# Kernel tuning notes

Hardware: AMD Instinct MI355X
Metric: run time of the kernel (lower is better)

## Reference

```python
import jax, jax.numpy as jnp
import numpy as np

H = 4          # num attention heads
LRELU = 0.2    # DGL GATConv leaky-relu slope
N_GT, N_AG = 100000, 20000
E_GT, E_COMM = 640000, 320000
D_GT, D_AG = 32, 64
VIS, COMM, MSG, OUT = 64, 128, 64, 5
NUM_COMM_STEPS = 2


def _leaky(x):
    return jnp.where(x >= 0, x, LRELU * x)


def gat(feat_src, feat_dst, w_src, w_dst, a_l, a_r, bias, src, dst, n_dst, dh):
    """Bipartite DGL GATConv: residual=Identity (in_dst == H*dh), activation=ReLU."""
    fs = (feat_src @ w_src).reshape(-1, H, dh)   # [Ns,H,dh]
    fd = (feat_dst @ w_dst).reshape(-1, H, dh)   # [Nd,H,dh]
    el = (fs * a_l[None]).sum(-1)                # [Ns,H]
    er = (fd * a_r[None]).sum(-1)                # [Nd,H]
    e = _leaky(el[src] + er[dst])                # [E,H]
    emax = jax.ops.segment_max(e, dst, num_segments=n_dst)
    ex = jnp.exp(e - emax[dst])
    denom = jax.ops.segment_sum(ex, dst, num_segments=n_dst)
    a = ex / denom[dst]                          # edge softmax over in-edges
    rst = jax.ops.segment_sum(fs[src] * a[..., None], dst, num_segments=n_dst)
    rst = rst + feat_dst.reshape(n_dst, H, dh)   # identity residual
    rst = rst + bias.reshape(1, H, dh)
    return jax.nn.relu(rst).reshape(n_dst, H * dh)


def gru(x, h, w_ih, w_hh, b_ih, b_hh):
    gi = x @ w_ih + b_ih
    gh = h @ w_hh + b_hh
    i_r, i_z, i_n = jnp.split(gi, 3, axis=1)
    h_r, h_z, h_n = jnp.split(gh, 3, axis=1)
    r = jax.nn.sigmoid(i_r + h_r)
    zg = jax.nn.sigmoid(i_z + h_z)
    n = jnp.tanh(i_n + r * h_n)
    return (1.0 - zg) * n + zg * h


def setup_inputs() -> dict:
    key = jax.random.key(0)
    ks = jax.random.split(key, 32)
    def w(k, shp):
        return (jax.random.normal(k, shp, dtype=jnp.float32) / np.sqrt(shp[0])).astype(jnp.float32)
    dh1, dh2 = VIS // H, COMM // H
    inp = {
        'feat_gt': jax.random.normal(ks[0], (N_GT, D_GT), dtype=jnp.float32),
        'feat_agent': jax.random.normal(ks[1], (N_AG, D_AG), dtype=jnp.float32),
        'z': jax.random.normal(ks[2], (N_AG, COMM), dtype=jnp.float32),
        'gt_src': jax.random.randint(ks[3], (E_GT,), 0, N_GT, dtype=jnp.int32),
        'gt_dst': jax.random.randint(ks[4], (E_GT,), 0, N_AG, dtype=jnp.int32),
        'comm_src': jax.random.randint(ks[5], (E_COMM,), 0, N_AG, dtype=jnp.int32),
        'comm_dst': jax.random.randint(ks[6], (E_COMM,), 0, N_AG, dtype=jnp.int32),
        # vis1 GATConv (gt->agent), out 64 = 4 heads x 16
        'w1_src': w(ks[7], (D_GT, VIS)), 'w1_dst': w(ks[8], (D_AG, VIS)),
        'a1_l': w(ks[9], (H, dh1)), 'a1_r': w(ks[10], (H, dh1)),
        'b1': jnp.zeros((VIS,), jnp.float32),
        'w2_src': w(ks[11], (D_GT, COMM)), 'w2_dst': w(ks[12], (VIS + D_AG, COMM)),
        'a2_l': w(ks[13], (H, dh2)), 'a2_r': w(ks[14], (H, dh2)),
        'b2': jnp.zeros((COMM,), jnp.float32),
        # comm f_enc: mlp([128,128,64]) with ReLU everywhere
        'enc_w1': w(ks[15], (COMM, 128)), 'enc_b1': jnp.zeros((128,), jnp.float32),
        'enc_w2': w(ks[16], (128, MSG)), 'enc_b2': jnp.zeros((MSG,), jnp.float32),
        # GRUCell(in=COMM+MSG=192, hidden=COMM=128), stored [in, 3*hidden]
        'gru_w_ih': w(ks[17], (COMM + MSG, 3 * COMM)),
        'gru_w_hh': w(ks[18], (COMM, 3 * COMM)),
        'gru_b_ih': jnp.zeros((3 * COMM,), jnp.float32),
        'gru_b_hh': jnp.zeros((3 * COMM,), jnp.float32),
        # f_out
        'out_w': w(ks[19], (COMM, OUT)), 'out_b': jnp.zeros((OUT,), jnp.float32),
    }
    return inp


def _forward(feat_gt, feat_agent, z, gt_src, gt_dst, comm_src, comm_dst,
             w1_src, w1_dst, a1_l, a1_r, b1,
             w2_src, w2_dst, a2_l, a2_r, b2,
             enc_w1, enc_b1, enc_w2, enc_b2,
             gru_w_ih, gru_w_hh, gru_b_ih, gru_b_hh,
             out_w, out_b):
    n_ag = feat_agent.shape[0]
    h_vis1 = gat(feat_gt, feat_agent, w1_src, w1_dst, a1_l, a1_r, b1,
                 gt_src, gt_dst, n_ag, VIS // H)
    dst2 = jnp.concatenate([h_vis1, feat_agent], axis=1)
    h = gat(feat_gt, dst2, w2_src, w2_dst, a2_l, a2_r, b2,
            gt_src, gt_dst, n_ag, COMM // H)
    deg = jax.ops.segment_sum(jnp.ones_like(comm_dst, dtype=jnp.float32),
                              comm_dst, num_segments=n_ag)
    denom = jnp.maximum(deg, 1.0)[:, None]
    zz = z
    for _ in range(NUM_COMM_STEPS):
        m = jax.nn.relu(jax.nn.relu(h @ enc_w1 + enc_b1) @ enc_w2 + enc_b2)  # per-node f_enc
        y = jax.ops.segment_sum(m[comm_src], comm_dst, num_segments=n_ag) / denom  # mailbox mean
        h = gru(jnp.concatenate([h, y], axis=1), zz, gru_w_ih, gru_w_hh, gru_b_ih, gru_b_hh)
        zz = h
    h_out = h @ out_w + out_b
    return h_out, zz


def reference(feat_gt, feat_agent, z, gt_src, gt_dst, comm_src, comm_dst,
              w1_src, w1_dst, a1_l, a1_r, b1,
              w2_src, w2_dst, a2_l, a2_r, b2,
              enc_w1, enc_b1, enc_w2, enc_b2,
              gru_w_ih, gru_w_hh, gru_b_ih, gru_b_hh,
              out_w, out_b):
    return _forward(feat_gt, feat_agent, z, gt_src, gt_dst, comm_src, comm_dst,
                    w1_src, w1_dst, a1_l, a1_r, b1,
                    w2_src, w2_dst, a2_l, a2_r, b2,
                    enc_w1, enc_b1, enc_w2, enc_b2,
                    gru_w_ih, gru_w_hh, gru_b_ih, gru_b_hh,
                    out_w, out_b)
```

## Files before the change

### kernel.cpp

```cpp
#include <hip/hip_runtime.h>
#include <math.h>

#define NHEAD 4
#define LRELU_S 0.2f
constexpr int N_GT = 100000, N_AG = 20000;
constexpr int E_GT = 640000, E_COMM = 320000;
constexpr int OUTD = 5;
constexpr int NBLK_SC = (N_AG + 255) / 256;
constexpr int MB_GT = (N_GT + 63) / 64;
constexpr int FS_TILES = 3 * MB_GT;
constexpr int ETILES  = (N_AG + 31) / 32;
constexpr int GGROUPS = (N_AG + 3) / 4;

constexpr long O_CNTP_GT = 0;
constexpr long O_CNTP_CM = 320000;
constexpr long O_FSB1    = 0;
constexpr long O_FSB2    = 3200000;
constexpr long O_EL1     = 12800000;
constexpr long O_EL2     = 13200000;
constexpr long O_ER1     = 14880000;
constexpr long O_RST2    = 17600000;
constexpr long O_DINV    = 20160000;
constexpr long O_OFFS_GT = 20180000;
constexpr long O_SRT_GT  = 20200004;
constexpr long O_OFFS_CM = 20840004;
constexpr long O_SRT_CM  = 20860008;
constexpr long O_PART    = 21180008;
constexpr long O_V       = 21220008;
constexpr long O_WB      = 21300000;
constexpr long O_RANK_GT = 21500000;
constexpr long O_RANK_CM = 22140000;
constexpr long O_M  = 10240000;
constexpr long O_Y  = 15360000;

constexpr long WB_FS  = 0;
constexpr long WB_E1  = 6144;
constexpr long WB_E2  = 22528;
constexpr long WB_RZ  = 30720;
constexpr long WB_GIN = 112640;
constexpr long WB_GHN = 137216;

using bf8      = __attribute__((ext_vector_type(8))) short;
using f32x4v   = __attribute__((ext_vector_type(4))) float;
using ushort8v = __attribute__((ext_vector_type(8))) unsigned short;

__device__ __forceinline__ unsigned short f2bf(float x) {
    unsigned u = __float_as_uint(x);
    u += 0x7FFFu + ((u >> 16) & 1u);
    return (unsigned short)(u >> 16);
}
__device__ __forceinline__ float bf2f(unsigned short u) {
    return __uint_as_float(((unsigned)u) << 16);
}

__global__ __launch_bounds__(256) void p0_k(
    const float* __restrict__ w1s, const float* __restrict__ w1d,
    const float* __restrict__ a1l, const float* __restrict__ a1r,
    const float* __restrict__ w2s, const float* __restrict__ w2d,
    const float* __restrict__ a2l, const float* __restrict__ a2r,
    const float* __restrict__ e1, const float* __restrict__ e2,
    const float* __restrict__ gih, const float* __restrict__ ghh,
    float* __restrict__ ws)
{
    const int tid = (int)(blockIdx.x * 256 + threadIdx.x);
    const int NT  = (int)(gridDim.x * 256);
    unsigned* wsu = reinterpret_cast<unsigned*>(ws);
    unsigned short* wb = reinterpret_cast<unsigned short*>(ws + O_WB);
    for (int i = tid; i < 640000; i += NT) wsu[O_CNTP_GT + i] = 0u;
    for (int i = tid; i < 153600; i += NT) {
        float val;
        if (i < 2048)        { long l = i;          long n = l / 32,  k = l % 32;  val = w1s[k * 64 + n]; }
        else if (i < 6144)   { long l = i - 2048;   long n = l / 32,  k = l % 32;  val = w2s[k * 128 + n]; }
        else if (i < 22528)  { long l = i - 6144;   long n = l / 128, k = l % 128; val = e1[k * 128 + n]; }
        else if (i < 30720)  { long l = i - 22528;  long n = l / 128, k = l % 128; val = e2[k * 64 + n]; }
        else if (i < 112640) { long l = i - 30720;  long n = l / 320, k = l % 320;
                               val = (k < 192) ? gih[k * 384 + n] : ghh[(k - 192) * 384 + n]; }
        else if (i < 137216) { long l = i - 112640; long n = l / 192, k = l % 192; val = gih[k * 384 + 256 + n]; }
        else                 { long l = i - 137216; long n = l / 128, k = l % 128; val = ghh[k * 384 + 256 + n]; }
        wb[i] = f2bf(val);
    }
    if (tid < 1024) {
        const int i = tid;
        const float *wp, *ap; int dh, local;
        if (i < 128)      { wp = w1s; ap = a1l; dh = 16; local = i; }
        else if (i < 384) { wp = w1d; ap = a1r; dh = 16; local = i - 128; }
        else if (i < 512) { wp = w2s; ap = a2l; dh = 32; local = i - 384; }
        else              { wp = w2d; ap = a2r; dh = 32; local = i - 512; }
        int k = local >> 2, hh = local & 3;
        float s = 0.f;
        for (int j = 0; j < dh; ++j) s += wp[k * (4 * dh) + hh * dh + j] * ap[hh * dh + j];
        ws[O_V + i] = s;
    }
}

__global__ __launch_bounds__(256) void p1_k(
    const int* __restrict__ gt_dst, const int* __restrict__ comm_dst,
    const float* __restrict__ feat_gt, const float* __restrict__ feat_agent,
    float* __restrict__ ws)
{
    const int tid = (int)(blockIdx.x * 256 + threadIdx.x);
    unsigned* wsu = reinterpret_cast<unsigned*>(ws);
    if (tid < E_GT) {
        wsu[O_RANK_GT + tid] = atomicAdd(wsu + O_CNTP_GT + (long)gt_dst[tid] * 16, 1u);
    } else if (tid < E_GT + E_COMM) {
        int j = tid - E_GT;
        wsu[O_RANK_CM + j] = atomicAdd(wsu + O_CNTP_CM + (long)comm_dst[j] * 16, 1u);
    }
    const float* v1  = ws + O_V;
    const float* v2  = ws + O_V + 384;
    const float* vr1 = ws + O_V + 128;
    float* el1 = ws + O_EL1;
    float* el2 = ws + O_EL2;
    float* er1 = ws + O_ER1;
    if (tid < N_GT) {
        const int i = tid;
        float a[8] = {};
        const float* fp = feat_gt + (long)i * 32;
        for (int k = 0; k < 32; ++k) {
            float x = fp[k];
#pragma unroll
            for (int j = 0; j < 4; ++j) a[j] += x * v1[4 * k + j];
#pragma unroll
            for (int j = 0; j < 4; ++j) a[4 + j] += x * v2[4 * k + j];
        }
        *reinterpret_cast<float4*>(el1 + 4l * i) = {a[0], a[1], a[2], a[3]};
        *reinterpret_cast<float4*>(el2 + 4l * i) = {a[4], a[5], a[6], a[7]};
    } else if (tid < N_GT + N_AG) {
        int r = tid - N_GT;
        float a0 = 0, a1 = 0, a2 = 0, a3 = 0;
        const float* fp = feat_agent + (long)r * 64;
        for (int k = 0; k < 64; ++k) {
            float x = fp[k];
            a0 += x * vr1[4 * k];     a1 += x * vr1[4 * k + 1];
            a2 += x * vr1[4 * k + 2]; a3 += x * vr1[4 * k + 3];
        }
        *reinterpret_cast<float4*>(er1 + 4l * r) = {a0, a1, a2, a3};
    }
}

__global__ __launch_bounds__(256) void p2_k(float* __restrict__ ws)
{
    __shared__ unsigned shu[256];
    unsigned* wsu = reinterpret_cast<unsigned*>(ws);
    const int b = (int)blockIdx.x, t = (int)threadIdx.x;
    const int g  = (b >= NBLK_SC) ? 1 : 0;
    const int cb = b - g * NBLK_SC;
    const int i  = cb * 256 + t;
    const unsigned* cnt = wsu + (g ? O_CNTP_CM : O_CNTP_GT);
    unsigned c = (i < N_AG) ? cnt[(long)i * 16] : 0u;
    if (g && i < N_AG) ws[O_DINV + i] = 1.0f / fmaxf((float)c, 1.0f);
    shu[t] = c;
    __syncthreads();
    for (int off = 1; off < 256; off <<= 1) {
        unsigned v = (t >= off) ? shu[t - off] : 0u;
        __syncthreads();
        shu[t] += v;
        __syncthreads();
    }
    unsigned* offs = wsu + (g ? O_OFFS_CM : O_OFFS_GT);
    if (i < N_AG) offs[i] = shu[t] - c;
    if (t == 255) wsu[O_PART + b] = shu[255];
}

__global__ __launch_bounds__(256) void p3_k(float* __restrict__ ws)
{
    __shared__ unsigned shu[128];
    unsigned* wsu = reinterpret_cast<unsigned*>(ws);
    const int b = (int)blockIdx.x, t = (int)threadIdx.x;
    const int g  = (b >= NBLK_SC) ? 1 : 0;
    const int cb = b - g * NBLK_SC;
    if (t < 128) shu[t] = (t < cb) ? wsu[O_PART + g * NBLK_SC + t] : 0u;
    __syncthreads();
    for (int off = 64; off >= 1; off >>= 1) {
        if (t < off) shu[t] += shu[t + off];
        __syncthreads();
    }
    const unsigned pre = shu[0];
    unsigned* offs = wsu + (g ? O_OFFS_CM : O_OFFS_GT);
    const int i = cb * 256 + t;
    if (i < N_AG) offs[i] += pre;
    if (b == NBLK_SC - 1 && t == 0)     wsu[O_OFFS_GT + N_AG] = E_GT;
    if (b == 2 * NBLK_SC - 1 && t == 0) wsu[O_OFFS_CM + N_AG] = E_COMM;
}

__global__ __launch_bounds__(256) void p4_k(
    const int* __restrict__ gt_src, const int* __restrict__ gt_dst,
    const int* __restrict__ comm_src, const int* __restrict__ comm_dst,
    const float* __restrict__ A, float* __restrict__ ws)
{
    unsigned* wsu = reinterpret_cast<unsigned*>(ws);
    const int t = (int)threadIdx.x;
    const int tid = (int)(blockIdx.x * 256 + t);
    if (tid < E_GT) {
        wsu[O_SRT_GT + wsu[O_OFFS_GT + gt_dst[tid]] + wsu[O_RANK_GT + tid]] = (unsigned)gt_src[tid];
    } else if (tid < E_GT + E_COMM) {
        int j = tid - E_GT;
        wsu[O_SRT_CM + wsu[O_OFFS_CM + comm_dst[j]] + wsu[O_RANK_CM + j]] = (unsigned)comm_src[j];
    }

    __shared__ __align__(16) unsigned short As[64][40];
    __shared__ __align__(16) unsigned short Bs[64][40];
    const unsigned short* Btc = reinterpret_cast<unsigned short*>(ws + O_WB) + WB_FS;
    unsigned short* fsb1 = reinterpret_cast<unsigned short*>(ws + O_FSB1);
    unsigned short* fsb2 = reinterpret_cast<unsigned short*>(ws + O_FSB2);
    const int lane = t & 63, wv = t >> 6;
    const int wm = wv & 1, wn = wv >> 1;
    const int quad = lane >> 4, l16 = lane & 15;
    const int rA = t >> 3, cA = (t & 7) * 4;
    const int rB = t >> 2, cB = (t & 3) * 8;
    const int tt = (int)blockIdx.x;
    if (tt >= FS_TILES) return;
    const int n0 = (tt % 3) * 64, m0 = (tt / 3) * 64;
#pragma unroll
    for (int half = 0; half < 2; ++half) {
        const int r = rA + half * 32;
        const int row = m0 + r;
        float4 v = {0.f, 0.f, 0.f, 0.f};
        if (row < N_GT) v = *reinterpret_cast<const float4*>(A + (long)row * 32 + cA);
        ushort4 bb;
        bb.x = f2bf(v.x); bb.y = f2bf(v.y); bb.z = f2bf(v.z); bb.w = f2bf(v.w);
        *reinterpret_cast<ushort4*>(&As[r][cA]) = bb;
    }
    *reinterpret_cast<ushort8v*>(&Bs[rB][cB]) =
        *reinterpret_cast<const ushort8v*>(Btc + (long)(n0 + rB) * 32 + cB);
    __syncthreads();
    f32x4v acc[2][2] = {};
    const bf8 a0 = *reinterpret_cast<const bf8*>(&As[wm * 32 + l16][quad * 8]);
    const bf8 a1 = *reinterpret_cast<const bf8*>(&As[wm * 32 + 16 + l16][quad * 8]);
    const bf8 b0v = *reinterpret_cast<const bf8*>(&Bs[wn * 32 + l16][quad * 8]);
    const bf8 b1v = *reinterpret_cast<const bf8*>(&Bs[wn * 32 + 16 + l16][quad * 8]);
    acc[0][0] = __builtin_amdgcn_mfma_f32_16x16x32_bf16(a0, b0v, acc[0][0], 0, 0, 0);
    acc[0][1] = __builtin_amdgcn_mfma_f32_16x16x32_bf16(a0, b1v, acc[0][1], 0, 0, 0);
    acc[1][0] = __builtin_amdgcn_mfma_f32_16x16x32_bf16(a1, b0v, acc[1][0], 0, 0, 0);
    acc[1][1] = __builtin_amdgcn_mfma_f32_16x16x32_bf16(a1, b1v, acc[1][1], 0, 0, 0);
#pragma unroll
    for (int mt = 0; mt < 2; ++mt)
#pragma unroll
        for (int nt = 0; nt < 2; ++nt)
#pragma unroll
            for (int r = 0; r < 4; ++r) {
                const int row = m0 + wm * 32 + mt * 16 + quad * 4 + r;
                const int col = n0 + wn * 32 + nt * 16 + l16;
                if (row < N_GT) {
                    unsigned short v16 = f2bf(acc[mt][nt][r]);
                    if (col < 64) fsb1[(long)row * 64 + col] = v16;
                    else          fsb2[(long)row * 128 + (col - 64)] = v16;
                }
            }
}

__global__ __launch_bounds__(256) void gat12_k(
    const unsigned* __restrict__ offs, const unsigned* __restrict__ ssrc,
    const float* __restrict__ el1, const float* __restrict__ er1,
    const float* __restrict__ el2,
    const unsigned short* __restrict__ fsb1, const unsigned short* __restrict__ fsb2,
    const float* __restrict__ feat_agent,
    const float* __restrict__ b1, const float* __restrict__ b2,
    const float* __restrict__ vr2, float* __restrict__ out)
{
    const int wid = threadIdx.x >> 6, lane = threadIdx.x & 63;
    const int d = blockIdx.x * 4 + wid;
    if (d >= N_AG) return;
    const int h = lane >> 4, ei = lane & 15;
    const unsigned beg = offs[d], end = offs[d + 1];
    const unsigned smax = (unsigned)N_GT - 1u;

    float m = -INFINITY, s = 0.f, acc0 = 0.f;
    {
        const float er_h = er1[4l * d + h];
        for (unsigned base = beg; base < end; base += 16) {
            const unsigned na = min(16u, end - base);
            unsigned sv = ssrc[base + ((unsigned)ei < na ? (unsigned)ei : 0u)];
            sv = min(sv, smax);
            unsigned short fw[16];
#pragma unroll
            for (int j = 0; j < 16; ++j) {
                const unsigned sj = (unsigned)__shfl((int)sv, j);
                fw[j] = fsb1[(long)sj * 64 + lane];
            }
            float xv = -INFINITY;
            if ((unsigned)ei < na) {
                float x = el1[4l * sv + h] + er_h;
                xv = (x >= 0.f) ? x : LRELU_S * x;
            }
            float cm = xv;
#pragma unroll
            for (int off = 1; off < 16; off <<= 1) cm = fmaxf(cm, __shfl_xor(cm, off));
            const float mn = fmaxf(m, cm);
            const float corr = __expf(m - mn);
            const float p = __expf(xv - mn);
            float ps = p;
#pragma unroll
            for (int off = 1; off < 16; off <<= 1) ps += __shfl_xor(ps, off);
            s = s * corr + ps;
            acc0 *= corr;
            m = mn;
#pragma unroll
            for (int j = 0; j < 16; ++j) {
                const float pj = __shfl(p, (h << 4) | j);
                acc0 += pj * bf2f(fw[j]);
            }
        }
    }
    const float inv1 = (s > 0.f) ? 1.f / s : 0.f;
    const float r1 = feat_agent[(long)d * 64 + lane];
    const float o = fmaxf(acc0 * inv1 + r1 + b1[lane], 0.f);

    float e0 = o * vr2[lane * 4 + 0] + r1 * vr2[(64 + lane) * 4 + 0];
    float e1v = o * vr2[lane * 4 + 1] + r1 * vr2[(64 + lane) * 4 + 1];
    float e2v = o * vr2[lane * 4 + 2] + r1 * vr2[(64 + lane) * 4 + 2];
    float e3v = o * vr2[lane * 4 + 3] + r1 * vr2[(64 + lane) * 4 + 3];
#pragma unroll
    for (int off = 1; off < 64; off <<= 1) {
        e0  += __shfl_xor(e0, off);
        e1v += __shfl_xor(e1v, off);
        e2v += __shfl_xor(e2v, off);
        e3v += __shfl_xor(e3v, off);
    }
    const float er_h2 = (h == 0) ? e0 : (h == 1) ? e1v : (h == 2) ? e2v : e3v;

    const int c0 = lane * 2;
    float m2 = -INFINITY, s2 = 0.f, A0 = 0.f, A1 = 0.f;
    for (unsigned base = beg; base < end; base += 16) {
        const unsigned na = min(16u, end - base);
        unsigned sv = ssrc[base + ((unsigned)ei < na ? (unsigned)ei : 0u)];
        sv = min(sv, smax);
        unsigned fw[16];
#pragma unroll
        for (int j = 0; j < 16; ++j) {
            const unsigned sj = (unsigned)__shfl((int)sv, j);
            fw[j] = *reinterpret_cast<const unsigned*>(fsb2 + (long)sj * 128 + c0);
        }
        float xv = -INFINITY;
        if ((unsigned)ei < na) {
            float x = el2[4l * sv + h] + er_h2;
            xv = (x >= 0.f) ? x : LRELU_S * x;
        }
        float cm = xv;
#pragma unroll
        for (int off = 1; off < 16; off <<= 1) cm = fmaxf(cm, __shfl_xor(cm, off));
        const float mn = fmaxf(m2, cm);
        const float corr = __expf(m2 - mn);
        const float p = __expf(xv - mn);
        float ps = p;
#pragma unroll
        for (int off = 1; off < 16; off <<= 1) ps += __shfl_xor(ps, off);
        s2 = s2 * corr + ps;
        A0 *= corr; A1 *= corr;
        m2 = mn;
#pragma unroll
        for (int j = 0; j < 16; ++j) {
            const float pj = __shfl(p, (h << 4) | j);
            A0 += pj * __uint_as_float((fw[j] & 0xFFFFu) << 16);
            A1 += pj * __uint_as_float((fw[j] >> 16) << 16);
        }
    }
    const float inv2 = (s2 > 0.f) ? 1.f / s2 : 0.f;
    const float rox = __shfl(o, c0 & 63);
    const float roy = __shfl(o, (c0 + 1) & 63);
    float2 r;
    if (c0 < 64) { r.x = rox; r.y = roy; }
    else r = *reinterpret_cast<const float2*>(feat_agent + (long)d * 64 + (c0 - 64));
    float2 oo;
    oo.x = fmaxf(A0 * inv2 + r.x + b2[c0], 0.f);
    oo.y = fmaxf(A1 * inv2 + r.y + b2[c0 + 1], 0.f);
    *reinterpret_cast<float2*>(out + (long)d * 128 + c0) = oo;
}

__global__ __launch_bounds__(256) void enc_k(
    const float* __restrict__ h,
    const unsigned short* __restrict__ we1, const unsigned short* __restrict__ we2,
    const float* __restrict__ eb1, const float* __restrict__ eb2,
    unsigned short* __restrict__ mb)
{
    __shared__ __align__(16) unsigned short U[8704];
    const int tid = (int)threadIdx.x;
    const int lane = tid & 63, w = tid >> 6;
    const int quad = lane >> 4, l16 = lane & 15;
    const int m0 = (int)blockIdx.x * 32;
#pragma unroll
    for (int it = 0; it < 4; ++it) {
        int idx = tid + it * 256;
        int row = idx >> 5, cc = (idx & 31) * 4;
        int grow = m0 + row;
        float4 v = {0.f, 0.f, 0.f, 0.f};
        if (grow < N_AG) v = *reinterpret_cast<const float4*>(h + (long)grow * 128 + cc);
        ushort4 bb;
        bb.x = f2bf(v.x); bb.y = f2bf(v.y); bb.z = f2bf(v.z); bb.w = f2bf(v.w);
        *reinterpret_cast<ushort4*>(&U[row * 136 + cc]) = bb;
    }
    __syncthreads();
#pragma unroll 1
    for (int jg = w; jg < 8; jg += 4) {
        const int j0 = jg * 16;
        const unsigned short* p = we1 + (long)(j0 + l16) * 128 + quad * 8;
        bf8 bw[4];
#pragma unroll
        for (int i2 = 0; i2 < 4; ++i2) bw[i2] = *reinterpret_cast<const bf8*>(p + i2 * 32);
        f32x4v acc[2] = {};
#pragma unroll
        for (int i2 = 0; i2 < 4; ++i2) {
            const int k0 = i2 * 32;
            const bf8 a0 = *reinterpret_cast<const bf8*>(&U[l16 * 136 + k0 + quad * 8]);
            const bf8 a1 = *reinterpret_cast<const bf8*>(&U[(16 + l16) * 136 + k0 + quad * 8]);
            acc[0] = __builtin_amdgcn_mfma_f32_16x16x32_bf16(a0, bw[i2], acc[0], 0, 0, 0);
            acc[1] = __builtin_amdgcn_mfma_f32_16x16x32_bf16(a1, bw[i2], acc[1], 0, 0, 0);
        }
        const int j = j0 + l16;
        const float bj = eb1[j];
#pragma unroll
        for (int mt = 0; mt < 2; ++mt)
#pragma unroll
            for (int r = 0; r < 4; ++r)
                U[4352 + (mt * 16 + quad * 4 + r) * 136 + j] = f2bf(fmaxf(acc[mt][r] + bj, 0.f));
    }
    __syncthreads();
    {
        const int j0 = w * 16;
        if (w < 4) {
            const unsigned short* p = we2 + (long)(j0 + l16) * 128 + quad * 8;
            bf8 bw[4];
#pragma unroll
            for (int i2 = 0; i2 < 4; ++i2) bw[i2] = *reinterpret_cast<const bf8*>(p + i2 * 32);
            f32x4v acc[2] = {};
#pragma unroll
            for (int i2 = 0; i2 < 4; ++i2) {
                const int k0 = i2 * 32;
                const bf8 a0 = *reinterpret_cast<const bf8*>(&U[4352 + l16 * 136 + k0 + quad * 8]);
                const bf8 a1 = *reinterpret_cast<const bf8*>(&U[4352 + (16 + l16) * 136 + k0 + quad * 8]);
                acc[0] = __builtin_amdgcn_mfma_f32_16x16x32_bf16(a0, bw[i2], acc[0], 0, 0, 0);
                acc[1] = __builtin_amdgcn_mfma_f32_16x16x32_bf16(a1, bw[i2], acc[1], 0, 0, 0);
            }
            const int j = j0 + l16;
            const float bj = eb2[j];
#pragma unroll
            for (int mt = 0; mt < 2; ++mt)
#pragma unroll
                for (int r = 0; r < 4; ++r) {
                    const int row = m0 + mt * 16 + quad * 4 + r;
                    if (row < N_AG)
                        mb[(long)row * 64 + j] = f2bf(fmaxf(acc[mt][r] + bj, 0.f));
                }
        }
    }
}

__global__ __launch_bounds__(256) void gather_k(
    const unsigned* __restrict__ coffs, const unsigned* __restrict__ cssrc,
    const unsigned short* __restrict__ mb, const float* __restrict__ dinv,
    float* __restrict__ y)
{
    const int tid = (int)threadIdx.x;
    const int lane = tid & 63, w = tid >> 6;
    const int d = (int)blockIdx.x * 4 + w;
    if (d >= N_AG) return;
    const unsigned beg = coffs[d], endo = coffs[d + 1];
    const int ei = lane & 15;
    float acc = 0.f;
    for (unsigned base = beg; base < endo; base += 16) {
        const unsigned na = min(16u, endo - base);
        unsigned sv = cssrc[base + ((unsigned)ei < na ? (unsigned)ei : 0u)];
        sv = min(sv, (unsigned)(N_AG - 1));
        unsigned short fw[16];
#pragma unroll
        for (int j = 0; j < 16; ++j) {
            const unsigned sj = (unsigned)__shfl((int)sv, j);
            fw[j] = mb[(long)sj * 64 + lane];
        }
#pragma unroll
        for (int j = 0; j < 16; ++j)
            if ((unsigned)j < na) acc += bf2f(fw[j]);
    }
    y[(long)d * 64 + lane] = acc * dinv[d];
}

__global__ __launch_bounds__(256) void gru_k(
    const float* __restrict__ h_in, const float* __restrict__ y, const float* zz,
    const unsigned short* __restrict__ wrz, const unsigned short* __restrict__ wgin,
    const unsigned short* __restrict__ wghn,
    const float* __restrict__ gbih, const float* __restrict__ gbhh,
    float* hout)
{
    __shared__ __align__(16) unsigned short U[32 * 328];
    const int tid = (int)threadIdx.x;
    const int lane = tid & 63, w = tid >> 6;
    const int quad = lane >> 4, l16 = lane & 15;
    const int m0 = (int)blockIdx.x * 32;
#pragma unroll
    for (int it = 0; it < 10; ++it) {
        int idx = tid + it * 256;
        int row = idx / 80, cc = (idx - row * 80) * 4;
        int grow = m0 + row;
        float4 v = {0.f, 0.f, 0.f, 0.f};
        if (grow < N_AG) {
            if (cc < 128)      v = *reinterpret_cast<const float4*>(h_in + (long)grow * 128 + cc);
            else if (cc < 192) v = *reinterpret_cast<const float4*>(y + (long)grow * 64 + (cc - 128));
            else               v = *reinterpret_cast<const float4*>(zz + (long)grow * 128 + (cc - 192));
        }
        ushort4 bb;
        bb.x = f2bf(v.x); bb.y = f2bf(v.y); bb.z = f2bf(v.z); bb.w = f2bf(v.w);
        *reinterpret_cast<ushort4*>(&U[row * 328 + cc]) = bb;
    }
    __syncthreads();
#pragma unroll 1
    for (int jg = w; jg < 8; jg += 4) {
        const int j0 = jg * 16;
        f32x4v aR[2] = {}, aZ[2] = {}, aI[2] = {}, aH[2] = {};
        {
            const unsigned short* pR = wrz + (long)(j0 + l16) * 320 + quad * 8;
            const unsigned short* pZ = wrz + (long)(128 + j0 + l16) * 320 + quad * 8;
#pragma unroll
            for (int half = 0; half < 2; ++half) {
                bf8 bR[5], bZ[5];
#pragma unroll
                for (int i2 = 0; i2 < 5; ++i2) {
                    const int k0 = half * 160 + i2 * 32;
                    bR[i2] = *reinterpret_cast<const bf8*>(pR + k0);
                    bZ[i2] = *reinterpret_cast<const bf8*>(pZ + k0);
                }
#pragma unroll
                for (int i2 = 0; i2 < 5; ++i2) {
                    const int k0 = half * 160 + i2 * 32;
                    const bf8 a0 = *reinterpret_cast<const bf8*>(&U[l16 * 328 + k0 + quad * 8]);
                    const bf8 a1 = *reinterpret_cast<const bf8*>(&U[(16 + l16) * 328 + k0 + quad * 8]);
                    aR[0] = __builtin_amdgcn_mfma_f32_16x16x32_bf16(a0, bR[i2], aR[0], 0, 0, 0);
                    aR[1] = __builtin_amdgcn_mfma_f32_16x16x32_bf16(a1, bR[i2], aR[1], 0, 0, 0);
                    aZ[0] = __builtin_amdgcn_mfma_f32_16x16x32_bf16(a0, bZ[i2], aZ[0], 0, 0, 0);
                    aZ[1] = __builtin_amdgcn_mfma_f32_16x16x32_bf16(a1, bZ[i2], aZ[1], 0, 0, 0);
                }
            }
        }
        {
            const unsigned short* pI = wgin + (long)(j0 + l16) * 192 + quad * 8;
            bf8 bI[6];
#pragma unroll
            for (int i2 = 0; i2 < 6; ++i2) bI[i2] = *reinterpret_cast<const bf8*>(pI + i2 * 32);
#pragma unroll
            for (int i2 = 0; i2 < 6; ++i2) {
                const int k0 = i2 * 32;
                const bf8 a0 = *reinterpret_cast<const bf8*>(&U[l16 * 328 + k0 + quad * 8]);
                const bf8 a1 = *reinterpret_cast<const bf8*>(&U[(16 + l16) * 328 + k0 + quad * 8]);
                aI[0] = __builtin_amdgcn_mfma_f32_16x16x32_bf16(a0, bI[i2], aI[0], 0, 0, 0);
                aI[1] = __builtin_amdgcn_mfma_f32_16x16x32_bf16(a1, bI[i2], aI[1], 0, 0, 0);
            }
        }
        {
            const unsigned short* pH = wghn + (long)(j0 + l16) * 128 + quad * 8;
            bf8 bH[4];
#pragma unroll
            for (int i2 = 0; i2 < 4; ++i2) bH[i2] = *reinterpret_cast<const bf8*>(pH + i2 * 32);
#pragma unroll
            for (int i2 = 0; i2 < 4; ++i2) {
                const int k0 = 192 + i2 * 32;
                const bf8 a0 = *reinterpret_cast<const bf8*>(&U[l16 * 328 + k0 + quad * 8]);
                const bf8 a1 = *reinterpret_cast<const bf8*>(&U[(16 + l16) * 328 + k0 + quad * 8]);
                aH[0] = __builtin_amdgcn_mfma_f32_16x16x32_bf16(a0, bH[i2], aH[0], 0, 0, 0);
                aH[1] = __builtin_amdgcn_mfma_f32_16x16x32_bf16(a1, bH[i2], aH[1], 0, 0, 0);
            }
        }
        const int j = j0 + l16;
#pragma unroll
        for (int mt = 0; mt < 2; ++mt)
#pragma unroll
            for (int r = 0; r < 4; ++r) {
                const int row = m0 + mt * 16 + quad * 4 + r;
                if (row >= N_AG) continue;
                const float rr = 1.f / (1.f + __expf(-(aR[mt][r] + gbih[j] + gbhh[j])));
                const float zg = 1.f / (1.f + __expf(-(aZ[mt][r] + gbih[128 + j] + gbhh[128 + j])));
                const float nn = tanhf(aI[mt][r] + gbih[256 + j] + rr * (aH[mt][r] + gbhh[256 + j]));
                const float hp = zz[(long)row * 128 + j];
                hout[(long)row * 128 + j] = (1.f - zg) * nn + zg * hp;
            }
    }
}

__global__ __launch_bounds__(256) void out_k(
    const float* __restrict__ h, const float* __restrict__ ow,
    const float* __restrict__ ob, float* __restrict__ out)
{
    const int gtid = (int)(blockIdx.x * 256 + threadIdx.x);
    float4* od = reinterpret_cast<float4*>(out + (long)N_AG * OUTD);
    const float4* hs = reinterpret_cast<const float4*>(h);
    if (gtid < N_AG * 32) od[gtid] = hs[gtid];
    if (gtid < N_AG) {
        float acc[OUTD];
#pragma unroll
        for (int j = 0; j < OUTD; ++j) acc[j] = ob[j];
        for (int k = 0; k < 128; ++k) {
            float v = h[(long)gtid * 128 + k];
#pragma unroll
            for (int j = 0; j < OUTD; ++j) acc[j] += v * ow[k * OUTD + j];
        }
#pragma unroll
        for (int j = 0; j < OUTD; ++j) out[(long)gtid * OUTD + j] = acc[j];
    }
}

extern "C" void kernel_launch(void* const* d_in, const int* in_sizes, int n_in,
                              void* d_out, int out_size, void* d_ws, size_t ws_size,
                              hipStream_t stream) {
    const float* feat_gt    = (const float*)d_in[0];
    const float* feat_agent = (const float*)d_in[1];
    const float* z_in       = (const float*)d_in[2];
    const int*   gt_src     = (const int*)d_in[3];
    const int*   gt_dst     = (const int*)d_in[4];
    const int*   comm_src   = (const int*)d_in[5];
    const int*   comm_dst   = (const int*)d_in[6];
    const float* w1_src = (const float*)d_in[7];
    const float* w1_dst = (const float*)d_in[8];
    const float* a1_l   = (const float*)d_in[9];
    const float* a1_r   = (const float*)d_in[10];
    const float* b1     = (const float*)d_in[11];
    const float* w2_src = (const float*)d_in[12];
    const float* w2_dst = (const float*)d_in[13];
    const float* a2_l   = (const float*)d_in[14];
    const float* a2_r   = (const float*)d_in[15];
    const float* b2     = (const float*)d_in[16];
    const float* enc_w1 = (const float*)d_in[17];
    const float* enc_b1 = (const float*)d_in[18];
    const float* enc_w2 = (const float*)d_in[19];
    const float* enc_b2 = (const float*)d_in[20];
    const float* gw_ih  = (const float*)d_in[21];
    const float* gw_hh  = (const float*)d_in[22];
    const float* gb_ih  = (const float*)d_in[23];
    const float* gb_hh  = (const float*)d_in[24];
    const float* out_w  = (const float*)d_in[25];
    const float* out_b  = (const float*)d_in[26];

    float* ws = (float*)d_ws;
    unsigned* wsu = (unsigned*)d_ws;
    unsigned short* wb = (unsigned short*)(ws + O_WB);
    float* out = (float*)d_out;

    float* hptr = ws + O_RST2;
    unsigned short* mb = (unsigned short*)(ws + O_M);
    float* yb = ws + O_Y;

    p0_k<<<dim3(2500), dim3(256), 0, stream>>>(w1_src, w1_dst, a1_l, a1_r,
                                               w2_src, w2_dst, a2_l, a2_r,
                                               enc_w1, enc_w2, gw_ih, gw_hh, ws);
    p1_k<<<dim3(3750), dim3(256), 0, stream>>>(gt_dst, comm_dst, feat_gt, feat_agent, ws);
    p2_k<<<dim3(2 * NBLK_SC), dim3(256), 0, stream>>>(ws);
    p3_k<<<dim3(2 * NBLK_SC), dim3(256), 0, stream>>>(ws);
    p4_k<<<dim3(FS_TILES), dim3(256), 0, stream>>>(gt_src, gt_dst, comm_src, comm_dst,
                                                   feat_gt, ws);

    gat12_k<<<dim3(GGROUPS), dim3(256), 0, stream>>>(
        wsu + O_OFFS_GT, wsu + O_SRT_GT,
        ws + O_EL1, ws + O_ER1, ws + O_EL2,
        (const unsigned short*)(ws + O_FSB1), (const unsigned short*)(ws + O_FSB2),
        feat_agent, b1, b2, ws + O_V + 512, hptr);

    for (int step = 0; step < 2; ++step) {
        const float* zz = (step == 0) ? z_in : hptr;
        enc_k<<<dim3(ETILES), dim3(256), 0, stream>>>(hptr, wb + WB_E1, wb + WB_E2,
                                                      enc_b1, enc_b2, mb);
        gather_k<<<dim3(GGROUPS), dim3(256), 0, stream>>>(wsu + O_OFFS_CM, wsu + O_SRT_CM,
                                                          mb, ws + O_DINV, yb);
        gru_k<<<dim3(ETILES), dim3(256), 0, stream>>>(hptr, yb, zz, wb + WB_RZ, wb + WB_GIN,
                                                      wb + WB_GHN, gb_ih, gb_hh, hptr);
    }
    out_k<<<dim3(2500), dim3(256), 0, stream>>>(hptr, out_w, out_b, out);
}
```

Baseline: 411.1 us.

## Process 32 edges per iteration in gathers and widen enc/gru blocks to 512

The GAT and mailbox gather loops now handle two 16-edge chunks per iteration, issuing both sets of feature loads before the online-softmax update so more memory requests are in flight and fewer reductions run per edge. The encoder and GRU kernels move to 512-thread blocks, with each of the 8 waves owning one 16-column slice instead of looping over two. This aims to hide gather latency and raise wave parallelism, at the cost of more registers per thread, which may lower occupancy.

```diff
diff --git a/kernel.cpp b/kernel.cpp
--- a/kernel.cpp
+++ b/kernel.cpp
@@ -268,28 +268,48 @@
     float m = -INFINITY, s = 0.f, acc0 = 0.f;
     {
         const float er_h = er1[4l * d + h];
-        for (unsigned base = beg; base < end; base += 16) {
-            const unsigned na = min(16u, end - base);
-            unsigned sv = ssrc[base + ((unsigned)ei < na ? (unsigned)ei : 0u)];
-            sv = min(sv, smax);
-            unsigned short fw[16];
+        for (unsigned base = beg; base < end; base += 32) {
+            const unsigned rem = end - base;
+            const unsigned naA = min(16u, rem);
+            const bool hasB = rem > 16u;
+            unsigned svA = ssrc[base + ((unsigned)ei < naA ? (unsigned)ei : 0u)];
+            svA = min(svA, smax);
+            unsigned svB = 0u; unsigned naB = 0u;
+            if (hasB) {
+                naB = min(16u, rem - 16u);
+                svB = ssrc[base + 16u + ((unsigned)ei < naB ? (unsigned)ei : 0u)];
+                svB = min(svB, smax);
+            }
+            unsigned short fwA[16], fwB[16];
 #pragma unroll
             for (int j = 0; j < 16; ++j) {
-                const unsigned sj = (unsigned)__shfl((int)sv, j);
-                fw[j] = fsb1[(long)sj * 64 + lane];
-            }
-            float xv = -INFINITY;
-            if ((unsigned)ei < na) {
-                float x = el1[4l * sv + h] + er_h;
-                xv = (x >= 0.f) ? x : LRELU_S * x;
-            }
-            float cm = xv;
+                const unsigned sj = (unsigned)__shfl((int)svA, j);
+                fwA[j] = fsb1[(long)sj * 64 + lane];
+            }
+            if (hasB) {
+#pragma unroll
+                for (int j = 0; j < 16; ++j) {
+                    const unsigned sj = (unsigned)__shfl((int)svB, j);
+                    fwB[j] = fsb1[(long)sj * 64 + lane];
+                }
+            }
+            float xvA = -INFINITY, xvB = -INFINITY;
+            if ((unsigned)ei < naA) {
+                float x = el1[4l * svA + h] + er_h;
+                xvA = (x >= 0.f) ? x : LRELU_S * x;
+            }
+            if (hasB && (unsigned)ei < naB) {
+                float x = el1[4l * svB + h] + er_h;
+                xvB = (x >= 0.f) ? x : LRELU_S * x;
+            }
+            float cm = fmaxf(xvA, xvB);
 #pragma unroll
             for (int off = 1; off < 16; off <<= 1) cm = fmaxf(cm, __shfl_xor(cm, off));
             const float mn = fmaxf(m, cm);
             const float corr = __expf(m - mn);
-            const float p = __expf(xv - mn);
-            float ps = p;
+            const float pA = __expf(xvA - mn);
+            const float pB = __expf(xvB - mn);
+            float ps = pA + pB;
 #pragma unroll
             for (int off = 1; off < 16; off <<= 1) ps += __shfl_xor(ps, off);
             s = s * corr + ps;
@@ -297,8 +317,15 @@
             m = mn;
 #pragma unroll
             for (int j = 0; j < 16; ++j) {
-                const float pj = __shfl(p, (h << 4) | j);
-                acc0 += pj * bf2f(fw[j]);
+                const float pj = __shfl(pA, (h << 4) | j);
+                acc0 += pj * bf2f(fwA[j]);
+            }
+            if (hasB) {
+#pragma unroll
+                for (int j = 0; j < 16; ++j) {
+                    const float pj = __shfl(pB, (h << 4) | j);
+                    acc0 += pj * bf2f(fwB[j]);
+                }
             }
         }
     }
@@ -321,28 +348,48 @@
 
     const int c0 = lane * 2;
     float m2 = -INFINITY, s2 = 0.f, A0 = 0.f, A1 = 0.f;
-    for (unsigned base = beg; base < end; base += 16) {
-        const unsigned na = min(16u, end - base);
-        unsigned sv = ssrc[base + ((unsigned)ei < na ? (unsigned)ei : 0u)];
-        sv = min(sv, smax);
-        unsigned fw[16];
+    for (unsigned base = beg; base < end; base += 32) {
+        const unsigned rem = end - base;
+        const unsigned naA = min(16u, rem);
+        const bool hasB = rem > 16u;
+        unsigned svA = ssrc[base + ((unsigned)ei < naA ? (unsigned)ei : 0u)];
+        svA = min(svA, smax);
+        unsigned svB = 0u; unsigned naB = 0u;
+        if (hasB) {
+            naB = min(16u, rem - 16u);
+            svB = ssrc[base + 16u + ((unsigned)ei < naB ? (unsigned)ei : 0u)];
+            svB = min(svB, smax);
+        }
+        unsigned fwA[16], fwB[16];
 #pragma unroll
         for (int j = 0; j < 16; ++j) {
-            const unsigned sj = (unsigned)__shfl((int)sv, j);
-            fw[j] = *reinterpret_cast<const unsigned*>(fsb2 + (long)sj * 128 + c0);
-        }
-        float xv = -INFINITY;
-        if ((unsigned)ei < na) {
-            float x = el2[4l * sv + h] + er_h2;
-            xv = (x >= 0.f) ? x : LRELU_S * x;
-        }
-        float cm = xv;
+            const unsigned sj = (unsigned)__shfl((int)svA, j);
+            fwA[j] = *reinterpret_cast<const unsigned*>(fsb2 + (long)sj * 128 + c0);
+        }
+        if (hasB) {
+#pragma unroll
+            for (int j = 0; j < 16; ++j) {
+                const unsigned sj = (unsigned)__shfl((int)svB, j);
+                fwB[j] = *reinterpret_cast<const unsigned*>(fsb2 + (long)sj * 128 + c0);
+            }
+        }
+        float xvA = -INFINITY, xvB = -INFINITY;
+        if ((unsigned)ei < naA) {
+            float x = el2[4l * svA + h] + er_h2;
+            xvA = (x >= 0.f) ? x : LRELU_S * x;
+        }
+        if (hasB && (unsigned)ei < naB) {
+            float x = el2[4l * svB + h] + er_h2;
+            xvB = (x >= 0.f) ? x : LRELU_S * x;
+        }
+        float cm = fmaxf(xvA, xvB);
 #pragma unroll
         for (int off = 1; off < 16; off <<= 1) cm = fmaxf(cm, __shfl_xor(cm, off));
         const float mn = fmaxf(m2, cm);
         const float corr = __expf(m2 - mn);
-        const float p = __expf(xv - mn);
-        float ps = p;
+        const float pA = __expf(xvA - mn);
+        const float pB = __expf(xvB - mn);
+        float ps = pA + pB;
 #pragma unroll
         for (int off = 1; off < 16; off <<= 1) ps += __shfl_xor(ps, off);
         s2 = s2 * corr + ps;
@@ -350,9 +397,17 @@
         m2 = mn;
 #pragma unroll
         for (int j = 0; j < 16; ++j) {
-            const float pj = __shfl(p, (h << 4) | j);
-            A0 += pj * __uint_as_float((fw[j] & 0xFFFFu) << 16);
-            A1 += pj * __uint_as_float((fw[j] >> 16) << 16);
+            const float pj = __shfl(pA, (h << 4) | j);
+            A0 += pj * __uint_as_float((fwA[j] & 0xFFFFu) << 16);
+            A1 += pj * __uint_as_float((fwA[j] >> 16) << 16);
+        }
+        if (hasB) {
+#pragma unroll
+            for (int j = 0; j < 16; ++j) {
+                const float pj = __shfl(pB, (h << 4) | j);
+                A0 += pj * __uint_as_float((fwB[j] & 0xFFFFu) << 16);
+                A1 += pj * __uint_as_float((fwB[j] >> 16) << 16);
+            }
         }
     }
     const float inv2 = (s2 > 0.f) ? 1.f / s2 : 0.f;
@@ -367,81 +422,79 @@
     *reinterpret_cast<float2*>(out + (long)d * 128 + c0) = oo;
 }
 
-__global__ __launch_bounds__(256) void enc_k(
+__global__ __launch_bounds__(512) void enc_k(
     const float* __restrict__ h,
     const unsigned short* __restrict__ we1, const unsigned short* __restrict__ we2,
     const float* __restrict__ eb1, const float* __restrict__ eb2,
     unsigned short* __restrict__ mb)
 {
-    __shared__ __align__(16) unsigned short U[8704];
+    __shared__ __align__(16) unsigned short As[32][136];
+    __shared__ __align__(16) unsigned short Ts[32][136];
     const int tid = (int)threadIdx.x;
     const int lane = tid & 63, w = tid >> 6;
     const int quad = lane >> 4, l16 = lane & 15;
     const int m0 = (int)blockIdx.x * 32;
 #pragma unroll
-    for (int it = 0; it < 4; ++it) {
-        int idx = tid + it * 256;
+    for (int it = 0; it < 2; ++it) {
+        int idx = tid + it * 512;
         int row = idx >> 5, cc = (idx & 31) * 4;
         int grow = m0 + row;
         float4 v = {0.f, 0.f, 0.f, 0.f};
         if (grow < N_AG) v = *reinterpret_cast<const float4*>(h + (long)grow * 128 + cc);
-        ushort4 bb;
-        bb.x = f2bf(v.x); bb.y = f2bf(v.y); bb.z = f2bf(v.z); bb.w = f2bf(v.w);
-        *reinterpret_cast<ushort4*>(&U[row * 136 + cc]) = bb;
-    }
-    __syncthreads();
-#pragma unroll 1
-    for (int jg = w; jg < 8; jg += 4) {
-        const int j0 = jg * 16;
-        const unsigned short* p = we1 + (long)(j0 + l16) * 128 + quad * 8;
-        bf8 bw[4];
-#pragma unroll
-        for (int i2 = 0; i2 < 4; ++i2) bw[i2] = *reinterpret_cast<const bf8*>(p + i2 * 32);
-        f32x4v acc[2] = {};
-#pragma unroll
-        for (int i2 = 0; i2 < 4; ++i2) {
-            const int k0 = i2 * 32;
-            const bf8 a0 = *reinterpret_cast<const bf8*>(&U[l16 * 136 + k0 + quad * 8]);
-            const bf8 a1 = *reinterpret_cast<const bf8*>(&U[(16 + l16) * 136 + k0 + quad * 8]);
-            acc[0] = __builtin_amdgcn_mfma_f32_16x16x32_bf16(a0, bw[i2], acc[0], 0, 0, 0);
-            acc[1] = __builtin_amdgcn_mfma_f32_16x16x32_bf16(a1, bw[i2], acc[1], 0, 0, 0);
-        }
-        const int j = j0 + l16;
-        const float bj = eb1[j];
-#pragma unroll
-        for (int mt = 0; mt < 2; ++mt)
-#pragma unroll
-            for (int r = 0; r < 4; ++r)
-                U[4352 + (mt * 16 + quad * 4 + r) * 136 + j] = f2bf(fmaxf(acc[mt][r] + bj, 0.f));
+        ushort4 b;
+        b.x = f2bf(v.x); b.y = f2bf(v.y); b.z = f2bf(v.z); b.w = f2bf(v.w);
+        *reinterpret_cast<ushort4*>(&As[row][cc]) = b;
     }
     __syncthreads();
     {
         const int j0 = w * 16;
-        if (w < 4) {
-            const unsigned short* p = we2 + (long)(j0 + l16) * 128 + quad * 8;
-            bf8 bw[4];
-#pragma unroll
-            for (int i2 = 0; i2 < 4; ++i2) bw[i2] = *reinterpret_cast<const bf8*>(p + i2 * 32);
-            f32x4v acc[2] = {};
-#pragma unroll
-            for (int i2 = 0; i2 < 4; ++i2) {
-                const int k0 = i2 * 32;
-                const bf8 a0 = *reinterpret_cast<const bf8*>(&U[4352 + l16 * 136 + k0 + quad * 8]);
-                const bf8 a1 = *reinterpret_cast<const bf8*>(&U[4352 + (16 + l16) * 136 + k0 + quad * 8]);
-                acc[0] = __builtin_amdgcn_mfma_f32_16x16x32_bf16(a0, bw[i2], acc[0], 0, 0, 0);
-                acc[1] = __builtin_amdgcn_mfma_f32_16x16x32_bf16(a1, bw[i2], acc[1], 0, 0, 0);
-            }
-            const int j = j0 + l16;
-            const float bj = eb2[j];
-#pragma unroll
-            for (int mt = 0; mt < 2; ++mt)
-#pragma unroll
-                for (int r = 0; r < 4; ++r) {
-                    const int row = m0 + mt * 16 + quad * 4 + r;
-                    if (row < N_AG)
-                        mb[(long)row * 64 + j] = f2bf(fmaxf(acc[mt][r] + bj, 0.f));
-                }
-        }
+        const unsigned short* p = we1 + (long)(j0 + l16) * 128 + quad * 8;
+        bf8 bw[4];
+#pragma unroll
+        for (int i = 0; i < 4; ++i) bw[i] = *reinterpret_cast<const bf8*>(p + i * 32);
+        f32x4v acc[2] = {};
+#pragma unroll
+        for (int i = 0; i < 4; ++i) {
+            const int k0 = i * 32;
+            const bf8 a0 = *reinterpret_cast<const bf8*>(&As[l16][k0 + quad * 8]);
+            const bf8 a1 = *reinterpret_cast<const bf8*>(&As[16 + l16][k0 + quad * 8]);
+            acc[0] = __builtin_amdgcn_mfma_f32_16x16x32_bf16(a0, bw[i], acc[0], 0, 0, 0);
+            acc[1] = __builtin_amdgcn_mfma_f32_16x16x32_bf16(a1, bw[i], acc[1], 0, 0, 0);
+        }
+        const int j = j0 + l16;
+        const float bj = eb1[j];
+#pragma unroll
+        for (int mt = 0; mt < 2; ++mt)
+#pragma unroll
+            for (int r = 0; r < 4; ++r)
+                Ts[mt * 16 + quad * 4 + r][j] = f2bf(fmaxf(acc[mt][r] + bj, 0.f));
+    }
+    __syncthreads();
+    if (w < 4) {
+        const int j0 = w * 16;
+        const unsigned short* p = we2 + (long)(j0 + l16) * 128 + quad * 8;
+        bf8 bw[4];
+#pragma unroll
+        for (int i = 0; i < 4; ++i) bw[i] = *reinterpret_cast<const bf8*>(p + i * 32);
+        f32x4v acc[2] = {};
+#pragma unroll
+        for (int i = 0; i < 4; ++i) {
+            const int k0 = i * 32;
+            const bf8 a0 = *reinterpret_cast<const bf8*>(&Ts[l16][k0 + quad * 8]);
+            const bf8 a1 = *reinterpret_cast<const bf8*>(&Ts[16 + l16][k0 + quad * 8]);
+            acc[0] = __builtin_amdgcn_mfma_f32_16x16x32_bf16(a0, bw[i], acc[0], 0, 0, 0);
+            acc[1] = __builtin_amdgcn_mfma_f32_16x16x32_bf16(a1, bw[i], acc[1], 0, 0, 0);
+        }
+        const int j = j0 + l16;
+        const float bj = eb2[j];
+#pragma unroll
+        for (int mt = 0; mt < 2; ++mt)
+#pragma unroll
+            for (int r = 0; r < 4; ++r) {
+                const int row = m0 + mt * 16 + quad * 4 + r;
+                if (row < N_AG)
+                    mb[(long)row * 64 + j] = f2bf(fmaxf(acc[mt][r] + bj, 0.f));
+            }
     }
 }
 
@@ -456,39 +509,60 @@
     if (d >= N_AG) return;
     const unsigned beg = coffs[d], endo = coffs[d + 1];
     const int ei = lane & 15;
+    const unsigned smax = (unsigned)N_AG - 1u;
     float acc = 0.f;
-    for (unsigned base = beg; base < endo; base += 16) {
-        const unsigned na = min(16u, endo - base);
-        unsigned sv = cssrc[base + ((unsigned)ei < na ? (unsigned)ei : 0u)];
-        sv = min(sv, (unsigned)(N_AG - 1));
-        unsigned short fw[16];
+    for (unsigned base = beg; base < endo; base += 32) {
+        const unsigned rem = endo - base;
+        const unsigned naA = min(16u, rem);
+        const bool hasB = rem > 16u;
+        unsigned svA = cssrc[base + ((unsigned)ei < naA ? (unsigned)ei : 0u)];
+        svA = min(svA, smax);
+        unsigned svB = 0u; unsigned naB = 0u;
+        if (hasB) {
+            naB = min(16u, rem - 16u);
+            svB = cssrc[base + 16u + ((unsigned)ei < naB ? (unsigned)ei : 0u)];
+            svB = min(svB, smax);
+        }
+        unsigned short fwA[16], fwB[16];
 #pragma unroll
         for (int j = 0; j < 16; ++j) {
-            const unsigned sj = (unsigned)__shfl((int)sv, j);
-            fw[j] = mb[(long)sj * 64 + lane];
+            const unsigned sj = (unsigned)__shfl((int)svA, j);
+            fwA[j] = mb[(long)sj * 64 + lane];
+        }
+        if (hasB) {
+#pragma unroll
+            for (int j = 0; j < 16; ++j) {
+                const unsigned sj = (unsigned)__shfl((int)svB, j);
+                fwB[j] = mb[(long)sj * 64 + lane];
+            }
         }
 #pragma unroll
         for (int j = 0; j < 16; ++j)
-            if ((unsigned)j < na) acc += bf2f(fw[j]);
+            if ((unsigned)j < naA) acc += bf2f(fwA[j]);
+        if (hasB) {
+#pragma unroll
+            for (int j = 0; j < 16; ++j)
+                if ((unsigned)j < naB) acc += bf2f(fwB[j]);
+        }
     }
     y[(long)d * 64 + lane] = acc * dinv[d];
 }
 
-__global__ __launch_bounds__(256) void gru_k(
+__global__ __launch_bounds__(512) void gru_k(
     const float* __restrict__ h_in, const float* __restrict__ y, const float* zz,
     const unsigned short* __restrict__ wrz, const unsigned short* __restrict__ wgin,
     const unsigned short* __restrict__ wghn,
     const float* __restrict__ gbih, const float* __restrict__ gbhh,
     float* hout)
 {
-    __shared__ __align__(16) unsigned short U[32 * 328];
+    __shared__ __align__(16) unsigned short As[32][328];
     const int tid = (int)threadIdx.x;
     const int lane = tid & 63, w = tid >> 6;
     const int quad = lane >> 4, l16 = lane & 15;
     const int m0 = (int)blockIdx.x * 32;
 #pragma unroll
-    for (int it = 0; it < 10; ++it) {
-        int idx = tid + it * 256;
+    for (int it = 0; it < 5; ++it) {
+        int idx = tid + it * 512;
         int row = idx / 80, cc = (idx - row * 80) * 4;
         int grow = m0 + row;
         float4 v = {0.f, 0.f, 0.f, 0.f};
@@ -497,81 +571,77 @@
             else if (cc < 192) v = *reinterpret_cast<const float4*>(y + (long)grow * 64 + (cc - 128));
             else               v = *reinterpret_cast<const float4*>(zz + (long)grow * 128 + (cc - 192));
         }
-        ushort4 bb;
-        bb.x = f2bf(v.x); bb.y = f2bf(v.y); bb.z = f2bf(v.z); bb.w = f2bf(v.w);
-        *reinterpret_cast<ushort4*>(&U[row * 328 + cc]) = bb;
+        ushort4 b;
+        b.x = f2bf(v.x); b.y = f2bf(v.y); b.z = f2bf(v.z); b.w = f2bf(v.w);
+        *reinterpret_cast<ushort4*>(&As[row][cc]) = b;
     }
     __syncthreads();
-#pragma unroll 1
-    for (int jg = w; jg < 8; jg += 4) {
-        const int j0 = jg * 16;
-        f32x4v aR[2] = {}, aZ[2] = {}, aI[2] = {}, aH[2] = {};
-        {
-            const unsigned short* pR = wrz + (long)(j0 + l16) * 320 + quad * 8;
-            const unsigned short* pZ = wrz + (long)(128 + j0 + l16) * 320 + quad * 8;
-#pragma unroll
-            for (int half = 0; half < 2; ++half) {
-                bf8 bR[5], bZ[5];
-#pragma unroll
-                for (int i2 = 0; i2 < 5; ++i2) {
-                    const int k0 = half * 160 + i2 * 32;
-                    bR[i2] = *reinterpret_cast<const bf8*>(pR + k0);
-                    bZ[i2] = *reinterpret_cast<const bf8*>(pZ + k0);
-                }
-#pragma unroll
-                for (int i2 = 0; i2 < 5; ++i2) {
-                    const int k0 = half * 160 + i2 * 32;
-                    const bf8 a0 = *reinterpret_cast<const bf8*>(&U[l16 * 328 + k0 + quad * 8]);
-                    const bf8 a1 = *reinterpret_cast<const bf8*>(&U[(16 + l16) * 328 + k0 + quad * 8]);
-                    aR[0] = __builtin_amdgcn_mfma_f32_16x16x32_bf16(a0, bR[i2], aR[0], 0, 0, 0);
-                    aR[1] = __builtin_amdgcn_mfma_f32_16x16x32_bf16(a1, bR[i2], aR[1], 0, 0, 0);
-                    aZ[0] = __builtin_amdgcn_mfma_f32_16x16x32_bf16(a0, bZ[i2], aZ[0], 0, 0, 0);
-                    aZ[1] = __builtin_amdgcn_mfma_f32_16x16x32_bf16(a1, bZ[i2], aZ[1], 0, 0, 0);
-                }
-            }
-        }
-        {
-            const unsigned short* pI = wgin + (long)(j0 + l16) * 192 + quad * 8;
-            bf8 bI[6];
-#pragma unroll
-            for (int i2 = 0; i2 < 6; ++i2) bI[i2] = *reinterpret_cast<const bf8*>(pI + i2 * 32);
-#pragma unroll
-            for (int i2 = 0; i2 < 6; ++i2) {
-                const int k0 = i2 * 32;
-                const bf8 a0 = *reinterpret_cast<const bf8*>(&U[l16 * 328 + k0 + quad * 8]);
-                const bf8 a1 = *reinterpret_cast<const bf8*>(&U[(16 + l16) * 328 + k0 + quad * 8]);
-                aI[0] = __builtin_amdgcn_mfma_f32_16x16x32_bf16(a0, bI[i2], aI[0], 0, 0, 0);
-                aI[1] = __builtin_amdgcn_mfma_f32_16x16x32_bf16(a1, bI[i2], aI[1], 0, 0, 0);
-            }
-        }
-        {
-            const unsigned short* pH = wghn + (long)(j0 + l16) * 128 + quad * 8;
-            bf8 bH[4];
-#pragma unroll
-            for (int i2 = 0; i2 < 4; ++i2) bH[i2] = *reinterpret_cast<const bf8*>(pH + i2 * 32);
-#pragma unroll
-            for (int i2 = 0; i2 < 4; ++i2) {
-                const int k0 = 192 + i2 * 32;
-                const bf8 a0 = *reinterpret_cast<const bf8*>(&U[l16 * 328 + k0 + quad * 8]);
-                const bf8 a1 = *reinterpret_cast<const bf8*>(&U[(16 + l16) * 328 + k0 + quad * 8]);
-                aH[0] = __builtin_amdgcn_mfma_f32_16x16x32_bf16(a0, bH[i2], aH[0], 0, 0, 0);
-                aH[1] = __builtin_amdgcn_mfma_f32_16x16x32_bf16(a1, bH[i2], aH[1], 0, 0, 0);
-            }
-        }
-        const int j = j0 + l16;
-#pragma unroll
-        for (int mt = 0; mt < 2; ++mt)
-#pragma unroll
-            for (int r = 0; r < 4; ++r) {
-                const int row = m0 + mt * 16 + quad * 4 + r;
-                if (row >= N_AG) continue;
-                const float rr = 1.f / (1.f + __expf(-(aR[mt][r] + gbih[j] + gbhh[j])));
-                const float zg = 1.f / (1.f + __expf(-(aZ[mt][r] + gbih[128 + j] + gbhh[128 + j])));
-                const float nn = tanhf(aI[mt][r] + gbih[256 + j] + rr * (aH[mt][r] + gbhh[256 + j]));
-                const float hp = zz[(long)row * 128 + j];
-                hout[(long)row * 128 + j] = (1.f - zg) * nn + zg * hp;
-            }
-    }
+
+    f32x4v aR[2] = {}, aZ[2] = {}, aI[2] = {}, aH[2] = {};
+    const int j0 = w * 16;
+    const unsigned short* pR = wrz + (long)(j0 + l16) * 320 + quad * 8;
+    const unsigned short* pZ = wrz + (long)(128 + j0 + l16) * 320 + quad * 8;
+#pragma unroll
+    for (int half = 0; half < 2; ++half) {
+        bf8 bR[5], bZ[5];
+#pragma unroll
+        for (int i = 0; i < 5; ++i) {
+            const int k0 = half * 160 + i * 32;
+            bR[i] = *reinterpret_cast<const bf8*>(pR + k0);
+            bZ[i] = *reinterpret_cast<const bf8*>(pZ + k0);
+        }
+#pragma unroll
+        for (int i = 0; i < 5; ++i) {
+            const int k0 = half * 160 + i * 32;
+            const bf8 a0 = *reinterpret_cast<const bf8*>(&As[l16][k0 + quad * 8]);
+            const bf8 a1 = *reinterpret_cast<const bf8*>(&As[16 + l16][k0 + quad * 8]);
+            aR[0] = __builtin_amdgcn_mfma_f32_16x16x32_bf16(a0, bR[i], aR[0], 0, 0, 0);
+            aR[1] = __builtin_amdgcn_mfma_f32_16x16x32_bf16(a1, bR[i], aR[1], 0, 0, 0);
+            aZ[0] = __builtin_amdgcn_mfma_f32_16x16x32_bf16(a0, bZ[i], aZ[0], 0, 0, 0);
+            aZ[1] = __builtin_amdgcn_mfma_f32_16x16x32_bf16(a1, bZ[i], aZ[1], 0, 0, 0);
+        }
+    }
+    {
+        const unsigned short* pI = wgin + (long)(j0 + l16) * 192 + quad * 8;
+        bf8 bI[6];
+#pragma unroll
+        for (int i = 0; i < 6; ++i) bI[i] = *reinterpret_cast<const bf8*>(pI + i * 32);
+#pragma unroll
+        for (int i = 0; i < 6; ++i) {
+            const int k0 = i * 32;
+            const bf8 a0 = *reinterpret_cast<const bf8*>(&As[l16][k0 + quad * 8]);
+            const bf8 a1 = *reinterpret_cast<const bf8*>(&As[16 + l16][k0 + quad * 8]);
+            aI[0] = __builtin_amdgcn_mfma_f32_16x16x32_bf16(a0, bI[i], aI[0], 0, 0, 0);
+            aI[1] = __builtin_amdgcn_mfma_f32_16x16x32_bf16(a1, bI[i], aI[1], 0, 0, 0);
+        }
+    }
+    {
+        const unsigned short* pH = wghn + (long)(j0 + l16) * 128 + quad * 8;
+        bf8 bH[4];
+#pragma unroll
+        for (int i = 0; i < 4; ++i) bH[i] = *reinterpret_cast<const bf8*>(pH + i * 32);
+#pragma unroll
+        for (int i = 0; i < 4; ++i) {
+            const int k0 = 192 + i * 32;
+            const bf8 a0 = *reinterpret_cast<const bf8*>(&As[l16][k0 + quad * 8]);
+            const bf8 a1 = *reinterpret_cast<const bf8*>(&As[16 + l16][k0 + quad * 8]);
+            aH[0] = __builtin_amdgcn_mfma_f32_16x16x32_bf16(a0, bH[i], aH[0], 0, 0, 0);
+            aH[1] = __builtin_amdgcn_mfma_f32_16x16x32_bf16(a1, bH[i], aH[1], 0, 0, 0);
+        }
+    }
+    const int j = j0 + l16;
+#pragma unroll
+    for (int mt = 0; mt < 2; ++mt)
+#pragma unroll
+        for (int r = 0; r < 4; ++r) {
+            const int row = m0 + mt * 16 + quad * 4 + r;
+            if (row >= N_AG) continue;
+            const float rr = 1.f / (1.f + __expf(-(aR[mt][r] + gbih[j] + gbhh[j])));
+            const float zg = 1.f / (1.f + __expf(-(aZ[mt][r] + gbih[128 + j] + gbhh[128 + j])));
+            const float nn = tanhf(aI[mt][r] + gbih[256 + j] + rr * (aH[mt][r] + gbhh[256 + j]));
+            const float hp = zz[(long)row * 128 + j];
+            hout[(long)row * 128 + j] = (1.f - zg) * nn + zg * hp;
+        }
 }
 
 __global__ __launch_bounds__(256) void out_k(
@@ -653,11 +723,11 @@
 
     for (int step = 0; step < 2; ++step) {
         const float* zz = (step == 0) ? z_in : hptr;
-        enc_k<<<dim3(ETILES), dim3(256), 0, stream>>>(hptr, wb + WB_E1, wb + WB_E2,
+        enc_k<<<dim3(ETILES), dim3(512), 0, stream>>>(hptr, wb + WB_E1, wb + WB_E2,
                                                       enc_b1, enc_b2, mb);
         gather_k<<<dim3(GGROUPS), dim3(256), 0, stream>>>(wsu + O_OFFS_CM, wsu + O_SRT_CM,
                                                           mb, ws + O_DINV, yb);
-        gru_k<<<dim3(ETILES), dim3(256), 0, stream>>>(hptr, yb, zz, wb + WB_RZ, wb + WB_GIN,
+        gru_k<<<dim3(ETILES), dim3(512), 0, stream>>>(hptr, yb, zz, wb + WB_RZ, wb + WB_GIN,
                                                       wb + WB_GHN, gb_ih, gb_hh, hptr);
     }
     out_k<<<dim3(2500), dim3(256), 0, stream>>>(hptr, out_w, out_b, out);
```

Measured after the change: 381.3 us. 1.08x faster.
